# Kernel optimization log

Hardware: AMD Instinct MI355X
Metric: run time of the kernel (lower is better)

The kernel has to match this reference:

```python
import jax, jax.numpy as jnp
import numpy as np

WINDOW_SIZE = 11
CHANNEL = 1
SIGMA = 1.5


def _gaussian_1d(size, sigma):
    coords = jnp.arange(size, dtype=jnp.float32) - size // 2
    g = jnp.exp(-coords ** 2 / (2 * sigma ** 2))
    return g / g.sum()


def _window_3d(size, channel, sigma=SIGMA):
    g = _gaussian_1d(size, sigma)
    w3 = g[:, None, None] * g[None, :, None] * g[None, None, :]  # [K,K,K]
    # OIDHW with groups=channel -> [channel, 1, K, K, K]
    return jnp.broadcast_to(w3[None, None], (channel, 1, size, size, size))


def _conv3d(x, window, channel):
    pad = WINDOW_SIZE // 2
    return jax.lax.conv_general_dilated(
        x, window,
        window_strides=(1, 1, 1),
        padding=[(pad, pad)] * 3,
        dimension_numbers=('NCDHW', 'OIDHW', 'NCDHW'),
        feature_group_count=channel,
    )


def setup_inputs() -> dict:
    key = jax.random.key(0)
    k1, k2 = jax.random.split(key)
    shape = (4, 1, 128, 128, 128)
    img1 = jax.random.uniform(k1, shape, dtype=jnp.float32)
    img2 = jax.random.uniform(k2, shape, dtype=jnp.float32)
    return {"img1": img1, "img2": img2}


def reference(img1, img2):
    channel = img1.shape[1]
    window = _window_3d(WINDOW_SIZE, channel).astype(img1.dtype)

    mu1 = _conv3d(img1, window, channel)
    mu2 = _conv3d(img2, window, channel)
    mu1_sq = mu1 * mu1
    mu2_sq = mu2 * mu2
    mu1_mu2 = mu1 * mu2

    sigma1_sq = _conv3d(img1 * img1, window, channel) - mu1_sq
    sigma2_sq = _conv3d(img2 * img2, window, channel) - mu2_sq
    sigma12 = _conv3d(img1 * img2, window, channel) - mu1_mu2

    C1 = 0.01 ** 2
    C2 = 0.03 ** 2
    ssim_map = ((2 * mu1_mu2 + C1) * (2 * sigma12 + C2)) / (
        (mu1_sq + mu2_sq + C1) * (sigma1_sq + sigma2_sq + C2))
    return ssim_map.mean()
```

## Files before the change

kernel.cpp:

```cpp
#include <hip/hip_runtime.h>
#include <hip/hip_fp16.h>
#include <math.h>

#define NB  4
#define DD  128
#define HH  128
#define WW  128
#define KS  11
#define PAD 5
#define NF  4
#define ZCK 32
#define HCK 32
#define RW  144

struct GW { float g[KS]; };

#define ZSTRIDE (HH * NF * WW)
#define HSTRIDE (NF * WW)

__global__ __launch_bounds__(256)
void k1_wd(const float* __restrict__ img1, const float* __restrict__ img2,
           __half* __restrict__ A, GW gw) {
    __shared__ float srow[2][2][2][RW];
    const int t  = threadIdx.x;
    const int b  = blockIdx.x;
    const int hb = b & 63;
    const int zc = (b >> 6) & 3;
    const int n  = b >> 8;
    const int r  = t >> 7;
    const int w  = t & 127;
    const int h  = hb * 2 + r;
    const int z0 = zc * ZCK;

    if (t < 80) {
        const int grp = t / 10;
        const int s10 = t % 10;
        const int slot = (s10 < 5) ? s10 : (WW + PAD + s10 - 5);
        srow[grp >> 2][(grp >> 1) & 1][grp & 1][slot] = 0.f;
    }

    const long long inBase = (long long)n * DD * HH * WW +
                             (long long)h * WW + w;
    const long long outBase = (long long)n * DD * ZSTRIDE +
                              (long long)h * HSTRIDE + w;

    float acc[NF][KS];
    #pragma unroll
    for (int f = 0; f < NF; ++f)
        #pragma unroll
        for (int j = 0; j < KS; ++j) acc[f][j] = 0.f;

    const int STEPS = ZCK + 2 * PAD;

    float rx0 = 0.f, ry0 = 0.f, rx1 = 0.f, ry1 = 0.f;
    {
        const int zi0 = z0 - PAD;
        if (zi0 >= 0) {
            const long long off = inBase + (long long)zi0 * (HH * WW);
            rx0 = img1[off]; ry0 = img2[off];
        }
        const int zi1 = z0 - PAD + 1;
        if (zi1 >= 0) {
            const long long off = inBase + (long long)zi1 * (HH * WW);
            rx1 = img1[off]; ry1 = img2[off];
        }
    }
    srow[0][0][r][PAD + w] = rx0;
    srow[0][1][r][PAD + w] = ry0;
    __syncthreads();

    #define K1_STEP(S, CUR, NXT, RXC, RYC, RXN, RYN, DOST)                     \
    {                                                                          \
        {              \
            const int zi = z0 - PAD + (S) + 2;                                 \
            float lx = 0.f, ly = 0.f;                                          \
            if ((S) + 2 < STEPS && zi >= 0 && zi < DD) {                       \
                const long long off = inBase + (long long)zi * (HH * WW);      \
                lx = img1[off]; ly = img2[off];                                \
            }                                                                  \
            RXC = lx; RYC = ly;                                                \
        }                                                                      \
                                    \
        float a0 = 0.f, a1 = 0.f, a2 = 0.f, a3 = 0.f;                          \
        _Pragma("unroll")                                                      \
        for (int k = 0; k < 5; ++k) {                                          \
            const float g  = gw.g[k];                                          \
            const float x0 = srow[CUR][0][r][w + k];                           \
            const float x1 = srow[CUR][0][r][w + 10 - k];                      \
            const float y0 = srow[CUR][1][r][w + k];                           \
            const float y1 = srow[CUR][1][r][w + 10 - k];                      \
            a0 = fmaf(g, x0 + x1, a0);                                         \
            a1 = fmaf(g, y0 + y1, a1);                                         \
            const float pxy = fmaf(x1, y1, x0 * y0);                           \
            a2 = fmaf(g, pxy, a2);                                             \
            float pss = x0 * x0;                                               \
            pss = fmaf(x1, x1, pss);                                           \
            pss = fmaf(y0, y0, pss);                                           \
            pss = fmaf(y1, y1, pss);                                           \
            a3 = fmaf(g, pss, a3);                                             \
        }                                                                      \
        {                                                                      \
            const float g = gw.g[5];                                           \
            const float x = srow[CUR][0][r][w + 5];                            \
            const float y = srow[CUR][1][r][w + 5];                            \
            a0 = fmaf(g, x, a0);                                               \
            a1 = fmaf(g, y, a1);                                               \
            a2 = fmaf(g, x * y, a2);                                           \
            const float ps = fmaf(y, y, x * x);                                \
            a3 = fmaf(g, ps, a3);                                              \
        }                                                                      \
                                             \
        srow[NXT][0][r][PAD + w] = RXN;                                        \
        srow[NXT][1][r][PAD + w] = RYN;                                        \
        __syncthreads();                                                       \
                                          \
        const float v[NF] = {a0, a1, a2, a3};                                  \
        _Pragma("unroll")                                                      \
        for (int f = 0; f < NF; ++f) {                                         \
            _Pragma("unroll")                                                  \
            for (int j = KS - 1; j >= 1; --j)                                  \
                acc[f][j] = fmaf(gw.g[j], v[f], acc[f][j - 1]);                \
            acc[f][0] = gw.g[0] * v[f];                                        \
        }                                                                      \
        if (DOST) {                                                            \
            const int zo = z0 + (S) - 2 * PAD;                                 \
            __half* op = A + outBase + (long long)zo * ZSTRIDE;                \
            op[0 * WW] = __float2half(acc[0][KS - 1]);                         \
            op[1 * WW] = __float2half(acc[1][KS - 1]);                         \
            op[2 * WW] = __float2half(acc[2][KS - 1]);                         \
            op[3 * WW] = __float2half(acc[3][KS - 1]);                         \
        }                                                                      \
    }

    for (int s2 = 0; s2 < 2 * PAD; s2 += 2) {
        K1_STEP(s2,     0, 1, rx0, ry0, rx1, ry1, 0)
        K1_STEP(s2 + 1, 1, 0, rx1, ry1, rx0, ry0, 0)
    }
    for (int s2 = 2 * PAD; s2 < STEPS; s2 += 2) {
        K1_STEP(s2,     0, 1, rx0, ry0, rx1, ry1, 1)
        K1_STEP(s2 + 1, 1, 0, rx1, ry1, rx0, ry0, 1)
    }
    #undef K1_STEP
}

__global__ __launch_bounds__(256)
void k2_hssim(const __half* __restrict__ A, double* __restrict__ partials,
              GW gw) {
    const int t  = threadIdx.x;
    const int b  = blockIdx.x;
    const int hc = b & 3;
    const int zp = (b >> 2) & 63;
    const int n  = b >> 8;
    const int zl = t >> 7;
    const int w  = t & 127;
    const int z  = zp * 2 + zl;
    const int h0 = hc * HCK;

    const long long colBase = ((long long)(n * DD + z)) * ZSTRIDE + w;

    float acc[NF][KS];
    #pragma unroll
    for (int f = 0; f < NF; ++f)
        #pragma unroll
        for (int j = 0; j < KS; ++j) acc[f][j] = 0.f;

    const int STEPS = HCK + 2 * PAD;

    __half pfA[NF], pfB[NF];
    #pragma unroll
    for (int f = 0; f < NF; ++f) { pfA[f] = __float2half(0.f); pfB[f] = pfA[f]; }
    {
        const int hi0 = h0 - PAD;
        if (hi0 >= 0) {
            const __half* p = A + colBase + (long long)hi0 * HSTRIDE;
            #pragma unroll
            for (int f = 0; f < NF; ++f) pfA[f] = p[f * WW];
        }
        const int hi1 = h0 - PAD + 1;
        if (hi1 >= 0) {
            const __half* p = A + colBase + (long long)hi1 * HSTRIDE;
            #pragma unroll
            for (int f = 0; f < NF; ++f) pfB[f] = p[f * WW];
        }
    }

    const float C1 = 1e-4f, C2 = 9e-4f;
    float sum = 0.f;

    #define K2_STEP(S, PFC, DOSSIM)                                            \
    {                                                                          \
        float v[NF];                                                           \
        _Pragma("unroll")                                                      \
        for (int f = 0; f < NF; ++f) v[f] = __half2float(PFC[f]);              \
        {                                       \
            const int hi = h0 - PAD + (S) + 2;                                 \
            _Pragma("unroll")                                                  \
            for (int f = 0; f < NF; ++f) PFC[f] = __float2half(0.f);           \
            if ((S) + 2 < STEPS && hi >= 0 && hi < HH) {                       \
                const __half* p = A + colBase + (long long)hi * HSTRIDE;       \
                _Pragma("unroll")                                              \
                for (int f = 0; f < NF; ++f) PFC[f] = p[f * WW];               \
            }                                                                  \
        }                                                                      \
        _Pragma("unroll")                                                      \
        for (int f = 0; f < NF; ++f) {                                         \
            _Pragma("unroll")                                                  \
            for (int j = KS - 1; j >= 1; --j)                                  \
                acc[f][j] = fmaf(gw.g[j], v[f], acc[f][j - 1]);                \
            acc[f][0] = gw.g[0] * v[f];                                        \
        }                                                                      \
        if (DOSSIM) {                                                          \
            const float mu1 = acc[0][KS - 1], mu2 = acc[1][KS - 1];            \
            const float mu1s = mu1 * mu1, mu2s = mu2 * mu2, mu12 = mu1 * mu2;  \
            const float sg12 = acc[2][KS - 1] - mu12;                          \
            const float sgss = acc[3][KS - 1] - mu1s - mu2s;                   \
            const float num = (2.f * mu12 + C1) * (2.f * sg12 + C2);           \
            const float den = (mu1s + mu2s + C1) * (sgss + C2);                \
            float rr = __builtin_amdgcn_rcpf(den);                             \
            rr = rr * fmaf(-den, rr, 2.0f);                     \
            sum = fmaf(num, rr, sum);                                          \
        }                                                                      \
    }

    for (int s2 = 0; s2 < 2 * PAD; s2 += 2) {
        K2_STEP(s2,     pfA, 0)
        K2_STEP(s2 + 1, pfB, 0)
    }
    for (int s2 = 2 * PAD; s2 < STEPS; s2 += 2) {
        K2_STEP(s2,     pfA, 1)
        K2_STEP(s2 + 1, pfB, 1)
    }
    #undef K2_STEP

    __shared__ double red[256];
    red[t] = (double)sum;
    __syncthreads();
    for (int sft = 128; sft > 0; sft >>= 1) {
        if (t < sft) red[t] += red[t + sft];
        __syncthreads();
    }
    if (t == 0) partials[b] = red[0];
}

__global__ __launch_bounds__(256)
void k4_reduce(const double* __restrict__ partials, int nPart,
               float* __restrict__ out) {
    __shared__ double red[256];
    const int t = threadIdx.x;
    double s = 0.0;
    for (int i = t; i < nPart; i += 256) s += partials[i];
    red[t] = s;
    __syncthreads();
    for (int sft = 128; sft > 0; sft >>= 1) {
        if (t < sft) red[t] += red[t + sft];
        __syncthreads();
    }
    if (t == 0) out[0] = (float)(red[0] / (double)((long long)NB * DD * HH * WW));
}

extern "C" void kernel_launch(void* const* d_in, const int* in_sizes, int n_in,
                              void* d_out, int out_size, void* d_ws, size_t ws_size,
                              hipStream_t stream) {
    const float* img1 = (const float*)d_in[0];
    const float* img2 = (const float*)d_in[1];
    float* out = (float*)d_out;

    GW gw;
    {
        double gs[KS], ssum = 0.0;
        for (int i = 0; i < KS; ++i) {
            const double c = (double)(i - KS / 2);
            gs[i] = exp(-c * c / (2.0 * 1.5 * 1.5));
            ssum += gs[i];
        }
        for (int i = 0; i < KS; ++i) gw.g[i] = (float)(gs[i] / ssum);
    }

    __half* A = (__half*)d_ws;
    double* partials =
        (double*)((char*)d_ws + (long long)NB * DD * ZSTRIDE * sizeof(__half));

    const int nBlocksK1 = NB * 64 * (DD / ZCK);
    const int nBlocksK2 = NB * 64 * (HH / HCK);

    k1_wd<<<nBlocksK1, 256, 0, stream>>>(img1, img2, A, gw);
    k2_hssim<<<nBlocksK2, 256, 0, stream>>>(A, partials, gw);
    k4_reduce<<<1, 256, 0, stream>>>(partials, nBlocksK2, out);
}
```

Before: 68.23 us.

## Process two W columns per thread with packed FP32 math and vector loads

Both the depth/width kernel and the height/SSIM kernel now give each thread two adjacent W columns. They use float2 and half2 loads and stores plus packed two-wide FMA vector types, and the per-block row or depth count doubles to keep 256 threads. The width convolution now precomputes products once per LDS element and runs a full 11-tap sum instead of the symmetric pairing. The aim is fewer load and store instructions and the use of packed FP32 FMA on CDNA. In exchange the grid is half the size and register pressure per thread roughly doubles because the accumulators grow to 88 floats, which may reduce occupancy.

```diff
diff --git a/kernel.cpp b/kernel.cpp
--- a/kernel.cpp
+++ b/kernel.cpp
@@ -12,8 +12,15 @@
 #define ZCK 32
 #define HCK 32
 #define RW  144
+#define LOFF 6
+
+using f32x2 = __attribute__((ext_vector_type(2))) float;
 
 struct GW { float g[KS]; };
+
+static __device__ __forceinline__ f32x2 vfma2(f32x2 a, f32x2 b, f32x2 c) {
+    return __builtin_elementwise_fma(a, b, c);
+}
 
 #define ZSTRIDE (HH * NF * WW)
 #define HSTRIDE (NF * WW)
@@ -21,114 +28,130 @@
 __global__ __launch_bounds__(256)
 void k1_wd(const float* __restrict__ img1, const float* __restrict__ img2,
            __half* __restrict__ A, GW gw) {
-    __shared__ float srow[2][2][2][RW];
+    __shared__ alignas(16) float srow[2][2][4][RW];
     const int t  = threadIdx.x;
     const int b  = blockIdx.x;
-    const int hb = b & 63;
-    const int zc = (b >> 6) & 3;
-    const int n  = b >> 8;
-    const int r  = t >> 7;
-    const int w  = t & 127;
-    const int h  = hb * 2 + r;
+    const int hb = b & 31;
+    const int zc = (b >> 5) & 3;
+    const int n  = b >> 7;
+    const int r  = t >> 6;
+    const int q  = t & 63;
+    const int w0 = q * 2;
+    const int h  = hb * 4 + r;
     const int z0 = zc * ZCK;
 
-    if (t < 80) {
-        const int grp = t / 10;
-        const int s10 = t % 10;
-        const int slot = (s10 < 5) ? s10 : (WW + PAD + s10 - 5);
-        srow[grp >> 2][(grp >> 1) & 1][grp & 1][slot] = 0.f;
-    }
-
-    const long long inBase = (long long)n * DD * HH * WW +
-                             (long long)h * WW + w;
+    if (t < 192) {
+        const int grp = t / 12, s12 = t % 12;
+        const int slot = (s12 < 6) ? s12 : (128 + s12);
+        srow[grp >> 3][(grp >> 2) & 1][grp & 3][slot] = 0.f;
+    }
+
+    const long long inBase  = (long long)n * DD * HH * WW +
+                              (long long)h * WW + w0;
     const long long outBase = (long long)n * DD * ZSTRIDE +
-                              (long long)h * HSTRIDE + w;
-
-    float acc[NF][KS];
+                              (long long)h * HSTRIDE + w0;
+
+    f32x2 acc[NF][KS];
     #pragma unroll
     for (int f = 0; f < NF; ++f)
         #pragma unroll
-        for (int j = 0; j < KS; ++j) acc[f][j] = 0.f;
+        for (int j = 0; j < KS; ++j) acc[f][j] = (f32x2){0.f, 0.f};
 
     const int STEPS = ZCK + 2 * PAD;
 
-    float rx0 = 0.f, ry0 = 0.f, rx1 = 0.f, ry1 = 0.f;
+    float2 rx0 = make_float2(0.f, 0.f), ry0 = rx0, rx1 = rx0, ry1 = rx0;
     {
         const int zi0 = z0 - PAD;
         if (zi0 >= 0) {
             const long long off = inBase + (long long)zi0 * (HH * WW);
-            rx0 = img1[off]; ry0 = img2[off];
+            rx0 = *(const float2*)(img1 + off);
+            ry0 = *(const float2*)(img2 + off);
         }
         const int zi1 = z0 - PAD + 1;
         if (zi1 >= 0) {
             const long long off = inBase + (long long)zi1 * (HH * WW);
-            rx1 = img1[off]; ry1 = img2[off];
-        }
-    }
-    srow[0][0][r][PAD + w] = rx0;
-    srow[0][1][r][PAD + w] = ry0;
+            rx1 = *(const float2*)(img1 + off);
+            ry1 = *(const float2*)(img2 + off);
+        }
+    }
+    *(float2*)&srow[0][0][r][LOFF + w0] = rx0;
+    *(float2*)&srow[0][1][r][LOFF + w0] = ry0;
     __syncthreads();
+
+    #define ELV(A2, i) ((i) & 1 ? A2[(i) >> 1].y : A2[(i) >> 1].x)
 
     #define K1_STEP(S, CUR, NXT, RXC, RYC, RXN, RYN, DOST)                     \
     {                                                                          \
-        {              \
+        {          \
             const int zi = z0 - PAD + (S) + 2;                                 \
-            float lx = 0.f, ly = 0.f;                                          \
+            float2 lx = make_float2(0.f, 0.f), ly = lx;                        \
             if ((S) + 2 < STEPS && zi >= 0 && zi < DD) {                       \
                 const long long off = inBase + (long long)zi * (HH * WW);      \
-                lx = img1[off]; ly = img2[off];                                \
+                lx = *(const float2*)(img1 + off);                             \
+                ly = *(const float2*)(img2 + off);                             \
             }                                                                  \
             RXC = lx; RYC = ly;                                                \
         }                                                                      \
+                  \
+        f32x2 xv2[7], yv2[7];                                                  \
+        _Pragma("unroll")                                                      \
+        for (int i = 0; i < 7; ++i) {                                          \
+            const float2 ax = *(const float2*)&srow[CUR][0][r][w0 + 2 * i];    \
+            const float2 ay = *(const float2*)&srow[CUR][1][r][w0 + 2 * i];    \
+            xv2[i] = (f32x2){ax.x, ax.y};                                      \
+            yv2[i] = (f32x2){ay.x, ay.y};                                      \
+        }                                                                      \
                                     \
-        float a0 = 0.f, a1 = 0.f, a2 = 0.f, a3 = 0.f;                          \
-        _Pragma("unroll")                                                      \
-        for (int k = 0; k < 5; ++k) {                                          \
-            const float g  = gw.g[k];                                          \
-            const float x0 = srow[CUR][0][r][w + k];                           \
-            const float x1 = srow[CUR][0][r][w + 10 - k];                      \
-            const float y0 = srow[CUR][1][r][w + k];                           \
-            const float y1 = srow[CUR][1][r][w + 10 - k];                      \
-            a0 = fmaf(g, x0 + x1, a0);                                         \
-            a1 = fmaf(g, y0 + y1, a1);                                         \
-            const float pxy = fmaf(x1, y1, x0 * y0);                           \
-            a2 = fmaf(g, pxy, a2);                                             \
-            float pss = x0 * x0;                                               \
-            pss = fmaf(x1, x1, pss);                                           \
-            pss = fmaf(y0, y0, pss);                                           \
-            pss = fmaf(y1, y1, pss);                                           \
-            a3 = fmaf(g, pss, a3);                                             \
-        }                                                                      \
-        {                                                                      \
-            const float g = gw.g[5];                                           \
-            const float x = srow[CUR][0][r][w + 5];                            \
-            const float y = srow[CUR][1][r][w + 5];                            \
-            a0 = fmaf(g, x, a0);                                               \
-            a1 = fmaf(g, y, a1);                                               \
-            a2 = fmaf(g, x * y, a2);                                           \
-            const float ps = fmaf(y, y, x * x);                                \
-            a3 = fmaf(g, ps, a3);                                              \
+        f32x2 pv2[7], qv2[7];                                                  \
+        _Pragma("unroll")                                                      \
+        for (int i = 0; i < 7; ++i) {                                          \
+            pv2[i] = xv2[i] * yv2[i];                                          \
+            qv2[i] = vfma2(yv2[i], yv2[i], xv2[i] * xv2[i]);                   \
+        }                                                                      \
+                            \
+        float a0x = 0.f, a0y = 0.f, a1x = 0.f, a1y = 0.f;                      \
+        float a2x = 0.f, a2y = 0.f, a3x = 0.f, a3y = 0.f;                      \
+        _Pragma("unroll")                                                      \
+        for (int k = 0; k < KS; ++k) {                                         \
+            const float g = gw.g[k];                                           \
+            a0x = fmaf(g, ELV(xv2, k + 1), a0x);                               \
+            a0y = fmaf(g, ELV(xv2, k + 2), a0y);                               \
+            a1x = fmaf(g, ELV(yv2, k + 1), a1x);                               \
+            a1y = fmaf(g, ELV(yv2, k + 2), a1y);                               \
+            a2x = fmaf(g, ELV(pv2, k + 1), a2x);                               \
+            a2y = fmaf(g, ELV(pv2, k + 2), a2y);                               \
+            a3x = fmaf(g, ELV(qv2, k + 1), a3x);                               \
+            a3y = fmaf(g, ELV(qv2, k + 2), a3y);                               \
         }                                                                      \
                                              \
-        srow[NXT][0][r][PAD + w] = RXN;                                        \
-        srow[NXT][1][r][PAD + w] = RYN;                                        \
+        *(float2*)&srow[NXT][0][r][LOFF + w0] = RXN;                           \
+        *(float2*)&srow[NXT][1][r][LOFF + w0] = RYN;                           \
         __syncthreads();                                                       \
-                                          \
-        const float v[NF] = {a0, a1, a2, a3};                                  \
+                                   \
+        f32x2 v[NF];                                                           \
+        v[0] = (f32x2){a0x, a0y}; v[1] = (f32x2){a1x, a1y};                    \
+        v[2] = (f32x2){a2x, a2y}; v[3] = (f32x2){a3x, a3y};                    \
         _Pragma("unroll")                                                      \
         for (int f = 0; f < NF; ++f) {                                         \
             _Pragma("unroll")                                                  \
-            for (int j = KS - 1; j >= 1; --j)                                  \
-                acc[f][j] = fmaf(gw.g[j], v[f], acc[f][j - 1]);                \
-            acc[f][0] = gw.g[0] * v[f];                                        \
+            for (int j = KS - 1; j >= 1; --j) {                                \
+                const f32x2 gg = {gw.g[j], gw.g[j]};                           \
+                acc[f][j] = vfma2(gg, v[f], acc[f][j - 1]);                    \
+            }                                                                  \
+            const f32x2 g0 = {gw.g[0], gw.g[0]};                               \
+            acc[f][0] = g0 * v[f];                                             \
         }                                                                      \
         if (DOST) {                                                            \
             const int zo = z0 + (S) - 2 * PAD;                                 \
             __half* op = A + outBase + (long long)zo * ZSTRIDE;                \
-            op[0 * WW] = __float2half(acc[0][KS - 1]);                         \
-            op[1 * WW] = __float2half(acc[1][KS - 1]);                         \
-            op[2 * WW] = __float2half(acc[2][KS - 1]);                         \
-            op[3 * WW] = __float2half(acc[3][KS - 1]);                         \
+            *(__half2*)(op + 0 * WW) =                                         \
+                __float22half2_rn(make_float2(acc[0][KS-1].x, acc[0][KS-1].y));\
+            *(__half2*)(op + 1 * WW) =                                         \
+                __float22half2_rn(make_float2(acc[1][KS-1].x, acc[1][KS-1].y));\
+            *(__half2*)(op + 2 * WW) =                                         \
+                __float22half2_rn(make_float2(acc[2][KS-1].x, acc[2][KS-1].y));\
+            *(__half2*)(op + 3 * WW) =                                         \
+                __float22half2_rn(make_float2(acc[3][KS-1].x, acc[3][KS-1].y));\
         }                                                                      \
     }
 
@@ -141,6 +164,7 @@
         K1_STEP(s2 + 1, 1, 0, rx1, ry1, rx0, ry0, 1)
     }
     #undef K1_STEP
+    #undef ELV
 }
 
 __global__ __launch_bounds__(256)
@@ -149,76 +173,86 @@
     const int t  = threadIdx.x;
     const int b  = blockIdx.x;
     const int hc = b & 3;
-    const int zp = (b >> 2) & 63;
-    const int n  = b >> 8;
-    const int zl = t >> 7;
-    const int w  = t & 127;
-    const int z  = zp * 2 + zl;
+    const int zp = (b >> 2) & 31;
+    const int n  = b >> 7;
+    const int zl = t >> 6;
+    const int q  = t & 63;
+    const int w0 = q * 2;
+    const int z  = zp * 4 + zl;
     const int h0 = hc * HCK;
 
-    const long long colBase = ((long long)(n * DD + z)) * ZSTRIDE + w;
-
-    float acc[NF][KS];
+    const long long colBase = ((long long)(n * DD + z)) * ZSTRIDE + w0;
+
+    f32x2 acc[NF][KS];
     #pragma unroll
     for (int f = 0; f < NF; ++f)
         #pragma unroll
-        for (int j = 0; j < KS; ++j) acc[f][j] = 0.f;
+        for (int j = 0; j < KS; ++j) acc[f][j] = (f32x2){0.f, 0.f};
 
     const int STEPS = HCK + 2 * PAD;
 
-    __half pfA[NF], pfB[NF];
-    #pragma unroll
-    for (int f = 0; f < NF; ++f) { pfA[f] = __float2half(0.f); pfB[f] = pfA[f]; }
+    unsigned pfA[NF] = {0u, 0u, 0u, 0u};
+    unsigned pfB[NF] = {0u, 0u, 0u, 0u};
     {
         const int hi0 = h0 - PAD;
         if (hi0 >= 0) {
             const __half* p = A + colBase + (long long)hi0 * HSTRIDE;
             #pragma unroll
-            for (int f = 0; f < NF; ++f) pfA[f] = p[f * WW];
+            for (int f = 0; f < NF; ++f) pfA[f] = *(const unsigned*)(p + f * WW);
         }
         const int hi1 = h0 - PAD + 1;
         if (hi1 >= 0) {
             const __half* p = A + colBase + (long long)hi1 * HSTRIDE;
             #pragma unroll
-            for (int f = 0; f < NF; ++f) pfB[f] = p[f * WW];
-        }
-    }
-
-    const float C1 = 1e-4f, C2 = 9e-4f;
-    float sum = 0.f;
+            for (int f = 0; f < NF; ++f) pfB[f] = *(const unsigned*)(p + f * WW);
+        }
+    }
+
+    const f32x2 C1v = {1e-4f, 1e-4f}, C2v = {9e-4f, 9e-4f};
+    const f32x2 TWO = {2.f, 2.f};
+    f32x2 sum = {0.f, 0.f};
 
     #define K2_STEP(S, PFC, DOSSIM)                                            \
     {                                                                          \
-        float v[NF];                                                           \
-        _Pragma("unroll")                                                      \
-        for (int f = 0; f < NF; ++f) v[f] = __half2float(PFC[f]);              \
-        {                                       \
+        f32x2 v[NF];                                                           \
+        _Pragma("unroll")                                                      \
+        for (int f = 0; f < NF; ++f) {                                         \
+            const float2 fv = __half22float2(*(const __half2*)&PFC[f]);        \
+            v[f] = (f32x2){fv.x, fv.y};                                        \
+        }                                                                      \
+        {                                                \
             const int hi = h0 - PAD + (S) + 2;                                 \
             _Pragma("unroll")                                                  \
-            for (int f = 0; f < NF; ++f) PFC[f] = __float2half(0.f);           \
+            for (int f = 0; f < NF; ++f) PFC[f] = 0u;                          \
             if ((S) + 2 < STEPS && hi >= 0 && hi < HH) {                       \
                 const __half* p = A + colBase + (long long)hi * HSTRIDE;       \
                 _Pragma("unroll")                                              \
-                for (int f = 0; f < NF; ++f) PFC[f] = p[f * WW];               \
+                for (int f = 0; f < NF; ++f)                                   \
+                    PFC[f] = *(const unsigned*)(p + f * WW);                   \
             }                                                                  \
         }                                                                      \
         _Pragma("unroll")                                                      \
         for (int f = 0; f < NF; ++f) {                                         \
             _Pragma("unroll")                                                  \
-            for (int j = KS - 1; j >= 1; --j)                                  \
-                acc[f][j] = fmaf(gw.g[j], v[f], acc[f][j - 1]);                \
-            acc[f][0] = gw.g[0] * v[f];                                        \
+            for (int j = KS - 1; j >= 1; --j) {                                \
+                const f32x2 gg = {gw.g[j], gw.g[j]};                           \
+                acc[f][j] = vfma2(gg, v[f], acc[f][j - 1]);                    \
+            }                                                                  \
+            const f32x2 g0 = {gw.g[0], gw.g[0]};                               \
+            acc[f][0] = g0 * v[f];                                             \
         }                                                                      \
         if (DOSSIM) {                                                          \
-            const float mu1 = acc[0][KS - 1], mu2 = acc[1][KS - 1];            \
-            const float mu1s = mu1 * mu1, mu2s = mu2 * mu2, mu12 = mu1 * mu2;  \
-            const float sg12 = acc[2][KS - 1] - mu12;                          \
-            const float sgss = acc[3][KS - 1] - mu1s - mu2s;                   \
-            const float num = (2.f * mu12 + C1) * (2.f * sg12 + C2);           \
-            const float den = (mu1s + mu2s + C1) * (sgss + C2);                \
-            float rr = __builtin_amdgcn_rcpf(den);                             \
-            rr = rr * fmaf(-den, rr, 2.0f);                     \
-            sum = fmaf(num, rr, sum);                                          \
+            const f32x2 mu1 = acc[0][KS - 1], mu2 = acc[1][KS - 1];            \
+            const f32x2 mu1s = mu1 * mu1, mu2s = mu2 * mu2, mu12 = mu1 * mu2;  \
+            const f32x2 sg12 = acc[2][KS - 1] - mu12;                          \
+            const f32x2 sgss = acc[3][KS - 1] - mu1s - mu2s;                   \
+            const f32x2 num = vfma2(TWO, mu12, C1v) * vfma2(TWO, sg12, C2v);   \
+            const f32x2 den = (mu1s + mu2s + C1v) * (sgss + C2v);              \
+            f32x2 rr;                                                          \
+            rr.x = __builtin_amdgcn_rcpf(den.x);                               \
+            rr.y = __builtin_amdgcn_rcpf(den.y);                               \
+            rr = rr * vfma2(-den, rr, TWO);                     \
+            sum = vfma2(num, rr, sum);                                         \
         }                                                                      \
     }
 
@@ -233,7 +267,7 @@
     #undef K2_STEP
 
     __shared__ double red[256];
-    red[t] = (double)sum;
+    red[t] = (double)sum.x + (double)sum.y;
     __syncthreads();
     for (int sft = 128; sft > 0; sft >>= 1) {
         if (t < sft) red[t] += red[t + sft];
@@ -280,8 +314,8 @@
     double* partials =
         (double*)((char*)d_ws + (long long)NB * DD * ZSTRIDE * sizeof(__half));
 
-    const int nBlocksK1 = NB * 64 * (DD / ZCK);
-    const int nBlocksK2 = NB * 64 * (HH / HCK);
+    const int nBlocksK1 = NB * 32 * (DD / ZCK);
+    const int nBlocksK2 = NB * 32 * (HH / HCK);
 
     k1_wd<<<nBlocksK1, 256, 0, stream>>>(img1, img2, A, gw);
     k2_hssim<<<nBlocksK2, 256, 0, stream>>>(A, partials, gw);
```

New measurement: 60.65 us. 11.1% less time.
